# Optimization experiments

Hardware: AMD Instinct MI355X
Metric: run time of the kernel (lower is better)

The kernel has to match this reference:

```python
import jax, jax.numpy as jnp
import numpy as np

HEADS = 16
DIM_HEAD = 64

def setup_inputs() -> dict:
    key = jax.random.key(0)
    ks = jax.random.split(key, 7)
    B, Nq, Dq = 4, 2048, 1024
    Nk, Dc = 1024, 768
    inner = HEADS * DIM_HEAD  # 1024
    sq = 1.0 / np.sqrt(Dq)
    sc = 1.0 / np.sqrt(Dc)
    si = 1.0 / np.sqrt(inner)
    return {
        "x": jax.random.normal(ks[0], (B, Nq, Dq), dtype=jnp.float32),
        "context": jax.random.normal(ks[1], (B, Nk, Dc), dtype=jnp.float32),
        "Wq": jax.random.normal(ks[2], (Dq, inner), dtype=jnp.float32) * sq,
        "Wk": jax.random.normal(ks[3], (Dc, inner), dtype=jnp.float32) * sc,
        "Wv": jax.random.normal(ks[4], (Dc, inner), dtype=jnp.float32) * sc,
        "Wo": jax.random.normal(ks[5], (inner, Dq), dtype=jnp.float32) * si,
        "bo": jax.random.normal(ks[6], (Dq,), dtype=jnp.float32) * 0.01,
    }

def reference(x, context, Wq, Wk, Wv, Wo, bo):
    B, Nq, _ = x.shape
    Nk = context.shape[1]
    h, dh = HEADS, DIM_HEAD
    # projections (no bias on q/k/v, matching nn.Linear(bias=False))
    q = (x @ Wq).reshape(B, Nq, h, dh)        # [B,Nq,h,dh]
    k = (context @ Wk).reshape(B, Nk, h, dh)  # [B,Nk,h,dh]
    v = (context @ Wv).reshape(B, Nk, h, dh)
    scale = 1.0 / jnp.sqrt(jnp.asarray(dh, dtype=x.dtype))
    # scores: [B,h,Nq,Nk]
    scores = jnp.einsum('bqhd,bkhd->bhqk', q, k) * scale
    attn = jax.nn.softmax(scores, axis=-1)
    out = jnp.einsum('bhqk,bkhd->bqhd', attn, v).reshape(B, Nq, h * dh)
    return out @ Wo + bo
```

## Files before the change

kernel.cpp:

```cpp
#include <hip/hip_runtime.h>

typedef __bf16 bf16;
typedef __bf16 bf16x2 __attribute__((ext_vector_type(2)));
typedef __bf16 bf16x4 __attribute__((ext_vector_type(4)));
typedef __bf16 bf16x8 __attribute__((ext_vector_type(8)));
typedef float f32x4 __attribute__((ext_vector_type(4)));

#define MFMA(a, b, c) __builtin_amdgcn_mfma_f32_16x16x32_bf16(a, b, c, 0, 0, 0)

#define GLD16(gptr, ldsptr)                                                        \
  __builtin_amdgcn_global_load_lds(                                                \
      (const __attribute__((address_space(1))) unsigned int*)(gptr),               \
      (__attribute__((address_space(3))) unsigned int*)(ldsptr), 16, 0, 0)

union I4B8 { int4 i; bf16x8 v; };
union HI { bf16x2 h; int i; };

__global__ __launch_bounds__(256) void prep_k(const float* __restrict__ x, bf16* __restrict__ xb,
                                              const float* __restrict__ ctx, bf16* __restrict__ ctxb,
                                              const float* __restrict__ Wq, bf16* __restrict__ WqT,
                                              const float* __restrict__ Wk, bf16* __restrict__ WkvT,
                                              const float* __restrict__ Wv,
                                              const float* __restrict__ Wo, bf16* __restrict__ WoT) {
  __shared__ float t[32][33];
  const int bid = blockIdx.x;
  if (bid < 5632) {
    const float* in; bf16* out; size_t i;
    if (bid < 4096) { in = x; out = xb; i = ((size_t)bid * 256 + threadIdx.x) * 8; }
    else { in = ctx; out = ctxb; i = ((size_t)(bid - 4096) * 256 + threadIdx.x) * 8; }
    const float4 a = *(const float4*)(in + i);
    const float4 b = *(const float4*)(in + i + 4);
    bf16x8 o;
    o[0] = (bf16)a.x; o[1] = (bf16)a.y; o[2] = (bf16)a.z; o[3] = (bf16)a.w;
    o[4] = (bf16)b.x; o[5] = (bf16)b.y; o[6] = (bf16)b.z; o[7] = (bf16)b.w;
    *(bf16x8*)(out + i) = o;
    return;
  }
  const int tt = bid - 5632;
  const int z = tt >> 10, rem = tt & 1023;
  const float* in; bf16* out; int R; float sc = 1.0f;
  if (z == 0)      { in = Wq; out = WqT;                R = 1024; sc = 0.18033688f; }
  else if (z == 1) { in = Wk; out = WkvT;               R = 768; }
  else if (z == 2) { in = Wv; out = WkvT + 1024 * 768;  R = 768; }
  else             { in = Wo; out = WoT;                R = 1024; }
  const int c0 = (rem & 31) * 32, r0 = (rem >> 5) * 32;
  if (r0 >= R) return;
  const int tx = threadIdx.x & 31, ty = threadIdx.x >> 5;
#pragma unroll
  for (int i = 0; i < 4; i++)
    t[ty + i * 8][tx] = in[(size_t)(r0 + ty + i * 8) * 1024 + c0 + tx];
  __syncthreads();
#pragma unroll
  for (int i = 0; i < 4; i++)
    out[(size_t)(c0 + ty + i * 8) * R + r0 + tx] = (bf16)(t[tx][ty + i * 8] * sc);
}

template <int MODE, int TN>
__device__ __forceinline__ void gemm_body(const bf16* __restrict__ A,
                                          const bf16* __restrict__ Bt,
                                          int K, int m0, int n0,
                                          void* __restrict__ C0,
                                          const float* __restrict__ bias,
                                          bf16* As, bf16* Bs) {
  constexpr int NI = TN / 32;
  const int tid = threadIdx.x;
  const int lane = tid & 63, wave = tid >> 6;
  const int wm = wave >> 1, wn = wave & 1;
  const int q = lane >> 4, c = lane & 15;

  f32x4 acc[4][NI] = {};
  const bf16* Ag = A + (size_t)(m0 + (tid >> 2)) * K + (tid & 3) * 8;
  const bf16* Bg = Bt + (size_t)(n0 + (tid >> 2)) * K + (tid & 3) * 8;
  const size_t K64 = (size_t)K * 64;
  bf16* AsW = &As[wave * 512];
  bf16* BsW = &Bs[wave * 512];

  for (int k0 = 0; k0 < K; k0 += 32) {
    __syncthreads();
    GLD16(Ag + k0, AsW);
    GLD16(Ag + k0 + K64, AsW + 2048);
    GLD16(Bg + k0, BsW);
    if constexpr (TN == 128) GLD16(Bg + k0 + K64, BsW + 2048);
    __syncthreads();
    bf16x8 af[4], bfr[NI];
#pragma unroll
    for (int mi = 0; mi < 4; mi++)
      af[mi] = *(const bf16x8*)&As[(wm * 64 + mi * 16 + c) * 32 + q * 8];
#pragma unroll
    for (int ni = 0; ni < NI; ni++)
      bfr[ni] = *(const bf16x8*)&Bs[(wn * (TN / 2) + ni * 16 + c) * 32 + q * 8];
#pragma unroll
    for (int mi = 0; mi < 4; mi++)
#pragma unroll
      for (int ni = 0; ni < NI; ni++) {
        if constexpr (MODE == 2)
          acc[mi][ni] = MFMA(af[mi], bfr[ni], acc[mi][ni]);
        else
          acc[mi][ni] = MFMA(bfr[ni], af[mi], acc[mi][ni]);
      }
  }

  if constexpr (MODE == 0 || MODE == 1) {
#pragma unroll
    for (int ni = 0; ni < NI; ni++) {
      const int col = n0 + wn * (TN / 2) + ni * 16 + q * 4;
      float4 bv4 = {};
      if constexpr (MODE == 1) bv4 = *(const float4*)&bias[col];
#pragma unroll
      for (int mi = 0; mi < 4; mi++) {
        const int row = m0 + wm * 64 + mi * 16 + c;
        if constexpr (MODE == 0) {
          bf16x4 vv;
#pragma unroll
          for (int r = 0; r < 4; r++) vv[r] = (bf16)acc[mi][ni][r];
          *(bf16x4*)&((bf16*)C0)[(size_t)row * 1024 + col] = vv;
        } else {
          f32x4 vv;
          vv[0] = acc[mi][ni][0] + bv4.x; vv[1] = acc[mi][ni][1] + bv4.y;
          vv[2] = acc[mi][ni][2] + bv4.z; vv[3] = acc[mi][ni][3] + bv4.w;
          *(f32x4*)&((float*)C0)[(size_t)row * 1024 + col] = vv;
        }
      }
    }
  } else {
#pragma unroll
    for (int ni = 0; ni < NI; ni++) {
      const int col = n0 + wn * (TN / 2) + ni * 16 + c;
#pragma unroll
      for (int mi = 0; mi < 4; mi++) {
        const int rbase = m0 + wm * 64 + mi * 16 + q * 4;
        const int b = rbase >> 10, key = rbase & 1023;
        bf16* VT = (bf16*)C0;
        const int h = col >> 6, d = col & 63;
        const int kl = key & 63;
        const int pkey = (key & ~63) | (kl & 32) | ((kl & 12) << 1) | ((kl & 16) >> 2);
        bf16x4 vv;
#pragma unroll
        for (int r = 0; r < 4; r++) vv[r] = (bf16)acc[mi][ni][r];
        *(bf16x4*)&VT[((size_t)(b * 16 + h) * 64 + d) * 1024 + pkey] = vv;
      }
    }
  }
}

__global__ __launch_bounds__(256) void proj_k(const bf16* __restrict__ xb,
                                              const bf16* __restrict__ ctxb,
                                              const bf16* __restrict__ WqT,
                                              const bf16* __restrict__ WkvT,
                                              bf16* __restrict__ Q,
                                              bf16* __restrict__ Kp,
                                              bf16* __restrict__ VT) {
  __shared__ __align__(16) bf16 As[4096];
  __shared__ __align__(16) bf16 Bs[4096];
  const int bid = blockIdx.x;
  if (bid < 512) {
    const int s = (bid & 7) * 64 + (bid >> 3);
    gemm_body<0, 128>(xb, WqT, 1024, (s >> 3) * 128, (s & 7) * 128, Q, nullptr, As, Bs);
  } else if (bid < 768) {
    const int t = bid - 512;
    const int s = (t & 7) * 32 + (t >> 3);
    gemm_body<0, 128>(ctxb, WkvT, 768, (s >> 3) * 128, (s & 7) * 128, Kp, nullptr, As, Bs);
  } else {
    const int t = bid - 768;
    const int s = (t & 7) * 32 + (t >> 3);
    gemm_body<2, 128>(ctxb, WkvT + (size_t)1024 * 768, 768, (s >> 3) * 128, (s & 7) * 128,
                      VT, nullptr, As, Bs);
  }
}

__global__ __launch_bounds__(256) void out_k(const bf16* __restrict__ O,
                                             const bf16* __restrict__ WoT,
                                             float* __restrict__ out,
                                             const float* __restrict__ bo) {
  __shared__ __align__(16) bf16 As[4096];
  __shared__ __align__(16) bf16 Bs[4096];
  const int bid = blockIdx.x;
  const int s = (bid & 7) * 64 + (bid >> 3);
  gemm_body<1, 128>(O, WoT, 1024, (s >> 3) * 128, (s & 7) * 128, out, bo, As, Bs);
}

__global__ __launch_bounds__(256) void attn_k(const bf16* __restrict__ Qg,
                                              const bf16* __restrict__ Kg,
                                              const bf16* __restrict__ VTg,
                                              bf16* __restrict__ Og) {
  __shared__ __align__(16) bf16 Ks[64][72];
  __shared__ __align__(16) bf16 Vt[64][72];
  const int tid = threadIdx.x;
  const int lane = tid & 63, w = tid >> 6;
  const int q = lane >> 4, c = lane & 15;
  const int bid = blockIdx.x;
  const int pair = (bid & 7) * 8 + (bid >> 7);
  const int head = pair & 15, b = pair >> 4;
  const int q0 = ((bid >> 3) & 15) * 128;

  bf16x8 aQ[2][2];
#pragma unroll
  for (int mj = 0; mj < 2; mj++)
#pragma unroll
    for (int ks = 0; ks < 2; ks++)
      aQ[mj][ks] = *(const bf16x8*)(Qg + (size_t)(b * 2048 + q0 + w * 32 + mj * 16 + c) * 1024 +
                                    head * 64 + ks * 32 + q * 8);

  f32x4 o[2][4] = {};
  f32x4 ol[2] = {};
  bf16x8 vone;
#pragma unroll
  for (int i = 0; i < 8; i++) vone[i] = (bf16)1.0f;

  const int srow = tid >> 2, sc = tid & 3;
  const bf16* Kbase = Kg + (size_t)(b * 1024 + srow) * 1024 + head * 64 + sc * 16;
  const bf16* Vbase = VTg + ((size_t)(b * 16 + head) * 64 + srow) * 1024 + sc * 16;

  bf16x8 rk0 = *(const bf16x8*)(Kbase);
  bf16x8 rk1 = *(const bf16x8*)(Kbase + 8);
  bf16x8 rv0 = *(const bf16x8*)(Vbase);
  bf16x8 rv1 = *(const bf16x8*)(Vbase + 8);

  for (int kt = 0; kt < 16; kt++) {
    __syncthreads();
    *(bf16x8*)&Ks[srow][sc * 16]     = rk0;
    *(bf16x8*)&Ks[srow][sc * 16 + 8] = rk1;
    *(bf16x8*)&Vt[srow][sc * 16]     = rv0;
    *(bf16x8*)&Vt[srow][sc * 16 + 8] = rv1;
    if (kt < 15) {
      const size_t ko = (size_t)(kt + 1) * 64 * 1024;
      const int vo = (kt + 1) * 64;
      rk0 = *(const bf16x8*)(Kbase + ko);
      rk1 = *(const bf16x8*)(Kbase + ko + 8);
      rv0 = *(const bf16x8*)(Vbase + vo);
      rv1 = *(const bf16x8*)(Vbase + vo + 8);
    }
    __syncthreads();

    f32x4 st[2][4] = {};
#pragma unroll
    for (int ks = 0; ks < 2; ks++) {
      bf16x8 ak[4];
#pragma unroll
      for (int ni = 0; ni < 4; ni++) ak[ni] = *(const bf16x8*)&Ks[ni * 16 + c][ks * 32 + q * 8];
      __builtin_amdgcn_s_setprio(1);
#pragma unroll
      for (int mj = 0; mj < 2; mj++)
#pragma unroll
        for (int ni = 0; ni < 4; ni++)
          st[mj][ni] = MFMA(ak[ni], aQ[mj][ks], st[mj][ni]);
      __builtin_amdgcn_s_setprio(0);
    }

    int pk[2][4][2];
#pragma unroll
    for (int mj = 0; mj < 2; mj++)
#pragma unroll
      for (int ni = 0; ni < 4; ni++) {
        float p0 = __builtin_amdgcn_exp2f(st[mj][ni][0]);
        float p1 = __builtin_amdgcn_exp2f(st[mj][ni][1]);
        float p2 = __builtin_amdgcn_exp2f(st[mj][ni][2]);
        float p3 = __builtin_amdgcn_exp2f(st[mj][ni][3]);
        HI h0, h1;
        h0.h[0] = (bf16)p0; h0.h[1] = (bf16)p1;
        h1.h[0] = (bf16)p2; h1.h[1] = (bf16)p3;
        pk[mj][ni][0] = h0.i;
        pk[mj][ni][1] = h1.i;
      }

#pragma unroll
    for (int ks2 = 0; ks2 < 2; ks2++) {
      bf16x8 bv[4];
#pragma unroll
      for (int ni = 0; ni < 4; ni++)
        bv[ni] = *(const bf16x8*)&Vt[ni * 16 + c][ks2 * 32 + q * 8];
#pragma unroll
      for (int mi = 0; mi < 2; mi++) {
        I4B8 pa;
        pa.i.x = pk[mi][2 * ks2][0];
        pa.i.y = pk[mi][2 * ks2][1];
        pa.i.z = pk[mi][2 * ks2 + 1][0];
        pa.i.w = pk[mi][2 * ks2 + 1][1];
        __builtin_amdgcn_s_setprio(1);
#pragma unroll
        for (int ni = 0; ni < 4; ni++)
          o[mi][ni] = MFMA(pa.v, bv[ni], o[mi][ni]);
        ol[mi] = MFMA(pa.v, vone, ol[mi]);
        __builtin_amdgcn_s_setprio(0);
      }
    }
  }

#pragma unroll
  for (int mi = 0; mi < 2; mi++) {
    float inv[4];
#pragma unroll
    for (int r = 0; r < 4; r++) inv[r] = 1.0f / ol[mi][r];
#pragma unroll
    for (int ni = 0; ni < 4; ni++)
#pragma unroll
      for (int r = 0; r < 4; r++) {
        const int qrow = q0 + w * 32 + mi * 16 + q * 4 + r;
        const int col = head * 64 + ni * 16 + c;
        Og[(size_t)(b * 2048 + qrow) * 1024 + col] = (bf16)(o[mi][ni][r] * inv[r]);
      }
  }
}

extern "C" void kernel_launch(void* const* d_in, const int* in_sizes, int n_in,
                              void* d_out, int out_size, void* d_ws, size_t ws_size,
                              hipStream_t stream) {
  (void)in_sizes; (void)n_in; (void)out_size; (void)ws_size;
  const float* x   = (const float*)d_in[0];
  const float* ctx = (const float*)d_in[1];
  const float* Wq  = (const float*)d_in[2];
  const float* Wk  = (const float*)d_in[3];
  const float* Wv  = (const float*)d_in[4];
  const float* Wo  = (const float*)d_in[5];
  const float* bo  = (const float*)d_in[6];
  float* out = (float*)d_out;

  char* ws = (char*)d_ws;
  const size_t MB = 1u << 20;
  bf16* WqT  = (bf16*)(ws);
  bf16* WkvT = (bf16*)(ws + 2 * MB);
  bf16* WoT  = (bf16*)(ws + 5 * MB);
  bf16* ctxb = (bf16*)(ws + 7 * MB);
  bf16* xb   = (bf16*)(ws + 13 * MB);
  bf16* Q    = (bf16*)(ws + 29 * MB);
  bf16* Kp   = (bf16*)(ws + 45 * MB);
  bf16* VT   = (bf16*)(ws + 53 * MB);
  bf16* O    = xb;

  prep_k<<<5632 + 4096, 256, 0, stream>>>(x, xb, ctx, ctxb, Wq, WqT, Wk, WkvT, Wv, Wo, WoT);

  proj_k<<<1024, 256, 0, stream>>>(xb, ctxb, WqT, WkvT, Q, Kp, VT);

  attn_k<<<1024, 256, 0, stream>>>(Q, Kp, VT, O);

  out_k<<<512, 256, 0, stream>>>(O, WoT, out, bo);
}
```

Measured before the change: 223.8 us.

## Deepen GEMM K-tile with XOR-swizzled LDS and load attention K/V directly from global

The projection and output GEMMs now stage a 64-wide K slice per iteration instead of 32, halving the number of barrier pairs, and use an XOR swizzle on the LDS columns to avoid bank conflicts. The MFMA block is wrapped in setprio. The attention kernel drops its LDS staging of K and V and the two barriers per tile, and instead has each wave read its MFMA fragments straight from global memory, relying on L2/L1 hits since every wave reads the same tiles. The risk is that the attention loop becomes exposed to global load latency with no software prefetch, and every wave issues redundant global loads.

```diff
diff --git a/kernel.cpp b/kernel.cpp
--- a/kernel.cpp
+++ b/kernel.cpp
@@ -55,55 +55,67 @@
     out[(size_t)(c0 + ty + i * 8) * R + r0 + tx] = (bf16)(t[tx][ty + i * 8] * sc);
 }
 
-template <int MODE, int TN>
+template <int MODE>
 __device__ __forceinline__ void gemm_body(const bf16* __restrict__ A,
                                           const bf16* __restrict__ Bt,
                                           int K, int m0, int n0,
                                           void* __restrict__ C0,
                                           const float* __restrict__ bias,
                                           bf16* As, bf16* Bs) {
-  constexpr int NI = TN / 32;
   const int tid = threadIdx.x;
   const int lane = tid & 63, wave = tid >> 6;
   const int wm = wave >> 1, wn = wave & 1;
   const int q = lane >> 4, c = lane & 15;
 
-  f32x4 acc[4][NI] = {};
-  const bf16* Ag = A + (size_t)(m0 + (tid >> 2)) * K + (tid & 3) * 8;
-  const bf16* Bg = Bt + (size_t)(n0 + (tid >> 2)) * K + (tid & 3) * 8;
-  const size_t K64 = (size_t)K * 64;
-  bf16* AsW = &As[wave * 512];
-  bf16* BsW = &Bs[wave * 512];
-
-  for (int k0 = 0; k0 < K; k0 += 32) {
+  f32x4 acc[4][4] = {};
+  const int r = tid >> 3;
+  const int col8 = ((tid & 7) * 8) ^ ((r & 7) * 8);
+  const bf16* Ag = A + (size_t)(m0 + r) * K + col8;
+  const bf16* Bg = Bt + (size_t)(n0 + r) * K + col8;
+  const size_t K32 = (size_t)K * 32;
+  bf16* AsW = As + wave * 512;
+  bf16* BsW = Bs + wave * 512;
+  const int swz = (c & 7) * 8;
+
+  for (int k0 = 0; k0 < K; k0 += 64) {
     __syncthreads();
-    GLD16(Ag + k0, AsW);
-    GLD16(Ag + k0 + K64, AsW + 2048);
-    GLD16(Bg + k0, BsW);
-    if constexpr (TN == 128) GLD16(Bg + k0 + K64, BsW + 2048);
+    GLD16(Ag + k0,            AsW);
+    GLD16(Ag + k0 + K32,      AsW + 2048);
+    GLD16(Ag + k0 + 2 * K32,  AsW + 4096);
+    GLD16(Ag + k0 + 3 * K32,  AsW + 6144);
+    GLD16(Bg + k0,            BsW);
+    GLD16(Bg + k0 + K32,      BsW + 2048);
+    GLD16(Bg + k0 + 2 * K32,  BsW + 4096);
+    GLD16(Bg + k0 + 3 * K32,  BsW + 6144);
     __syncthreads();
-    bf16x8 af[4], bfr[NI];
-#pragma unroll
-    for (int mi = 0; mi < 4; mi++)
-      af[mi] = *(const bf16x8*)&As[(wm * 64 + mi * 16 + c) * 32 + q * 8];
-#pragma unroll
-    for (int ni = 0; ni < NI; ni++)
-      bfr[ni] = *(const bf16x8*)&Bs[(wn * (TN / 2) + ni * 16 + c) * 32 + q * 8];
-#pragma unroll
-    for (int mi = 0; mi < 4; mi++)
-#pragma unroll
-      for (int ni = 0; ni < NI; ni++) {
-        if constexpr (MODE == 2)
-          acc[mi][ni] = MFMA(af[mi], bfr[ni], acc[mi][ni]);
-        else
-          acc[mi][ni] = MFMA(bfr[ni], af[mi], acc[mi][ni]);
-      }
+#pragma unroll
+    for (int kk = 0; kk < 2; kk++) {
+      const int cx = (kk * 32 + q * 8) ^ swz;
+      bf16x8 af[4], bfr[4];
+#pragma unroll
+      for (int mi = 0; mi < 4; mi++)
+        af[mi] = *(const bf16x8*)&As[(wm * 64 + mi * 16 + c) * 64 + cx];
+#pragma unroll
+      for (int ni = 0; ni < 4; ni++)
+        bfr[ni] = *(const bf16x8*)&Bs[(wn * 64 + ni * 16 + c) * 64 + cx];
+      __builtin_amdgcn_s_setprio(1);
+#pragma unroll
+      for (int mi = 0; mi < 4; mi++)
+#pragma unroll
+        for (int ni = 0; ni < 4; ni++) {
+          if constexpr (MODE == 2)
+            acc[mi][ni] = MFMA(af[mi], bfr[ni], acc[mi][ni]);
+          else
+            acc[mi][ni] = MFMA(bfr[ni], af[mi], acc[mi][ni]);
+        }
+      __builtin_amdgcn_s_setprio(0);
+    }
   }
 
   if constexpr (MODE == 0 || MODE == 1) {
 #pragma unroll
-    for (int ni = 0; ni < NI; ni++) {
-      const int col = n0 + wn * (TN / 2) + ni * 16 + q * 4;
+    for (int ni = 0; ni < 4; ni++) {
+      const int col = n0 + wn * 64 + ni * 16 + q * 4;
       float4 bv4 = {};
       if constexpr (MODE == 1) bv4 = *(const float4*)&bias[col];
 #pragma unroll
@@ -112,7 +124,7 @@
         if constexpr (MODE == 0) {
           bf16x4 vv;
 #pragma unroll
-          for (int r = 0; r < 4; r++) vv[r] = (bf16)acc[mi][ni][r];
+          for (int r2 = 0; r2 < 4; r2++) vv[r2] = (bf16)acc[mi][ni][r2];
           *(bf16x4*)&((bf16*)C0)[(size_t)row * 1024 + col] = vv;
         } else {
           f32x4 vv;
@@ -124,8 +136,8 @@
     }
   } else {
 #pragma unroll
-    for (int ni = 0; ni < NI; ni++) {
-      const int col = n0 + wn * (TN / 2) + ni * 16 + c;
+    for (int ni = 0; ni < 4; ni++) {
+      const int col = n0 + wn * 64 + ni * 16 + c;
 #pragma unroll
       for (int mi = 0; mi < 4; mi++) {
         const int rbase = m0 + wm * 64 + mi * 16 + q * 4;
@@ -136,7 +148,7 @@
         const int pkey = (key & ~63) | (kl & 32) | ((kl & 12) << 1) | ((kl & 16) >> 2);
         bf16x4 vv;
 #pragma unroll
-        for (int r = 0; r < 4; r++) vv[r] = (bf16)acc[mi][ni][r];
+        for (int r2 = 0; r2 < 4; r2++) vv[r2] = (bf16)acc[mi][ni][r2];
         *(bf16x4*)&VT[((size_t)(b * 16 + h) * 64 + d) * 1024 + pkey] = vv;
       }
     }
@@ -150,21 +162,21 @@
                                               bf16* __restrict__ Q,
                                               bf16* __restrict__ Kp,
                                               bf16* __restrict__ VT) {
-  __shared__ __align__(16) bf16 As[4096];
-  __shared__ __align__(16) bf16 Bs[4096];
+  __shared__ __align__(16) bf16 As[8192];
+  __shared__ __align__(16) bf16 Bs[8192];
   const int bid = blockIdx.x;
   if (bid < 512) {
     const int s = (bid & 7) * 64 + (bid >> 3);
-    gemm_body<0, 128>(xb, WqT, 1024, (s >> 3) * 128, (s & 7) * 128, Q, nullptr, As, Bs);
+    gemm_body<0>(xb, WqT, 1024, (s >> 3) * 128, (s & 7) * 128, Q, nullptr, As, Bs);
   } else if (bid < 768) {
     const int t = bid - 512;
     const int s = (t & 7) * 32 + (t >> 3);
-    gemm_body<0, 128>(ctxb, WkvT, 768, (s >> 3) * 128, (s & 7) * 128, Kp, nullptr, As, Bs);
+    gemm_body<0>(ctxb, WkvT, 768, (s >> 3) * 128, (s & 7) * 128, Kp, nullptr, As, Bs);
   } else {
     const int t = bid - 768;
     const int s = (t & 7) * 32 + (t >> 3);
-    gemm_body<2, 128>(ctxb, WkvT + (size_t)1024 * 768, 768, (s >> 3) * 128, (s & 7) * 128,
-                      VT, nullptr, As, Bs);
+    gemm_body<2>(ctxb, WkvT + (size_t)1024 * 768, 768, (s >> 3) * 128, (s & 7) * 128,
+                 VT, nullptr, As, Bs);
   }
 }
 
@@ -172,19 +184,17 @@
                                              const bf16* __restrict__ WoT,
                                              float* __restrict__ out,
                                              const float* __restrict__ bo) {
-  __shared__ __align__(16) bf16 As[4096];
-  __shared__ __align__(16) bf16 Bs[4096];
+  __shared__ __align__(16) bf16 As[8192];
+  __shared__ __align__(16) bf16 Bs[8192];
   const int bid = blockIdx.x;
   const int s = (bid & 7) * 64 + (bid >> 3);
-  gemm_body<1, 128>(O, WoT, 1024, (s >> 3) * 128, (s & 7) * 128, out, bo, As, Bs);
+  gemm_body<1>(O, WoT, 1024, (s >> 3) * 128, (s & 7) * 128, out, bo, As, Bs);
 }
 
 __global__ __launch_bounds__(256) void attn_k(const bf16* __restrict__ Qg,
                                               const bf16* __restrict__ Kg,
                                               const bf16* __restrict__ VTg,
                                               bf16* __restrict__ Og) {
-  __shared__ __align__(16) bf16 Ks[64][72];
-  __shared__ __align__(16) bf16 Vt[64][72];
   const int tid = threadIdx.x;
   const int lane = tid & 63, w = tid >> 6;
   const int q = lane >> 4, c = lane & 15;
@@ -207,45 +217,37 @@
 #pragma unroll
   for (int i = 0; i < 8; i++) vone[i] = (bf16)1.0f;
 
-  const int srow = tid >> 2, sc = tid & 3;
-  const bf16* Kbase = Kg + (size_t)(b * 1024 + srow) * 1024 + head * 64 + sc * 16;
-  const bf16* Vbase = VTg + ((size_t)(b * 16 + head) * 64 + srow) * 1024 + sc * 16;
-
-  bf16x8 rk0 = *(const bf16x8*)(Kbase);
-  bf16x8 rk1 = *(const bf16x8*)(Kbase + 8);
-  bf16x8 rv0 = *(const bf16x8*)(Vbase);
-  bf16x8 rv1 = *(const bf16x8*)(Vbase + 8);
-
+  const bf16* Kf = Kg + (size_t)(b * 1024 + c) * 1024 + head * 64 + q * 8;
+  const bf16* Vf = VTg + ((size_t)(b * 16 + head) * 64 + c) * 1024 + q * 8;
+
+#pragma unroll 1
   for (int kt = 0; kt < 16; kt++) {
-    __syncthreads();
-    *(bf16x8*)&Ks[srow][sc * 16]     = rk0;
-    *(bf16x8*)&Ks[srow][sc * 16 + 8] = rk1;
-    *(bf16x8*)&Vt[srow][sc * 16]     = rv0;
-    *(bf16x8*)&Vt[srow][sc * 16 + 8] = rv1;
-    if (kt < 15) {
-      const size_t ko = (size_t)(kt + 1) * 64 * 1024;
-      const int vo = (kt + 1) * 64;
-      rk0 = *(const bf16x8*)(Kbase + ko);
-      rk1 = *(const bf16x8*)(Kbase + ko + 8);
-      rv0 = *(const bf16x8*)(Vbase + vo);
-      rv1 = *(const bf16x8*)(Vbase + vo + 8);
-    }
-    __syncthreads();
+    const bf16* Kt = Kf + (size_t)kt * 65536;
+    bf16x8 ak[2][4];
+#pragma unroll
+    for (int ks = 0; ks < 2; ks++)
+#pragma unroll
+      for (int ni = 0; ni < 4; ni++)
+        ak[ks][ni] = *(const bf16x8*)(Kt + ni * 16384 + ks * 32);
 
     f32x4 st[2][4] = {};
-#pragma unroll
-    for (int ks = 0; ks < 2; ks++) {
-      bf16x8 ak[4];
-#pragma unroll
-      for (int ni = 0; ni < 4; ni++) ak[ni] = *(const bf16x8*)&Ks[ni * 16 + c][ks * 32 + q * 8];
-      __builtin_amdgcn_s_setprio(1);
+    __builtin_amdgcn_s_setprio(1);
+#pragma unroll
+    for (int ks = 0; ks < 2; ks++)
 #pragma unroll
       for (int mj = 0; mj < 2; mj++)
 #pragma unroll
         for (int ni = 0; ni < 4; ni++)
-          st[mj][ni] = MFMA(ak[ni], aQ[mj][ks], st[mj][ni]);
-      __builtin_amdgcn_s_setprio(0);
-    }
+          st[mj][ni] = MFMA(ak[ks][ni], aQ[mj][ks], st[mj][ni]);
+    __builtin_amdgcn_s_setprio(0);
+
+    const bf16* Vt2 = Vf + kt * 64;
+    bf16x8 bv[2][4];
+#pragma unroll
+    for (int ks2 = 0; ks2 < 2; ks2++)
+#pragma unroll
+      for (int ni = 0; ni < 4; ni++)
+        bv[ks2][ni] = *(const bf16x8*)(Vt2 + ni * 16384 + ks2 * 32);
 
     int pk[2][4][2];
 #pragma unroll
@@ -265,10 +267,6 @@
 
 #pragma unroll
     for (int ks2 = 0; ks2 < 2; ks2++) {
-      bf16x8 bv[4];
-#pragma unroll
-      for (int ni = 0; ni < 4; ni++)
-        bv[ni] = *(const bf16x8*)&Vt[ni * 16 + c][ks2 * 32 + q * 8];
 #pragma unroll
       for (int mi = 0; mi < 2; mi++) {
         I4B8 pa;
@@ -279,7 +277,7 @@
         __builtin_amdgcn_s_setprio(1);
 #pragma unroll
         for (int ni = 0; ni < 4; ni++)
-          o[mi][ni] = MFMA(pa.v, bv[ni], o[mi][ni]);
+          o[mi][ni] = MFMA(pa.v, bv[ks2][ni], o[mi][ni]);
         ol[mi] = MFMA(pa.v, vone, ol[mi]);
         __builtin_amdgcn_s_setprio(0);
       }
```

Result: slower. 313.9 us (+40.2%).
